# Performance work log

Measured on AMD Instinct MI355X. Metric: run time of the kernel, lower is better.

Reference implementation:

```python
import jax, jax.numpy as jnp
import numpy as np

I_P = 8  # input_patch == output_patch


def extract_patches(x, i_p=I_P):
    # x: (B, N, C, H, W) -> (r, N*i_p*i_p, B, C), matching nn.Unfold(i_p, 1, 0, i_p)
    # followed by rearrange '(b n) (c i) r -> r (n i) b c' with i = h*w row-major.
    B, N, C, H, W = x.shape
    s1, s2 = H // i_p, W // i_p
    p = x.reshape(B, N, C, s1, i_p, s2, i_p)
    p = jnp.transpose(p, (3, 5, 1, 4, 6, 0, 2))  # (s1, s2, N, ph, pw, B, C)
    return p.reshape(s1 * s2, N * i_p * i_p, B, C)


def setup_inputs() -> dict:
    key = jax.random.key(0)
    ks = jax.random.split(key, 8)
    B, N, C, H = 1, 5, 3, 256
    inputs = jax.random.normal(ks[0], (B, N, C, H, H), jnp.float32)
    outputs = jax.random.normal(ks[1], (B, N, C, H, H), jnp.float32)
    # q/k projections of nn.MultiheadAttention(3, 1); v_proj and out_proj are frozen identity.
    Wq = jax.random.normal(ks[2], (3, 3), jnp.float32) * 0.5
    Wk = jax.random.normal(ks[3], (3, 3), jnp.float32) * 0.5
    bq = jax.random.normal(ks[4], (3,), jnp.float32) * 0.05
    bk = jax.random.normal(ks[5], (3,), jnp.float32) * 0.05
    bv = jnp.zeros((3,), jnp.float32)  # in_proj_bias for v initialised to zero
    return {
        "inputs": inputs,
        "outputs": outputs,
        "Wq": Wq,
        "Wk": Wk,
        "bq": bq,
        "bk": bk,
        "bv": bv,
        "loss_diff": jnp.float32(0.5),
        "step": 10,
        "max_steps": 100,
    }


def reference(inputs, outputs, Wq, Wk, bq, bk, bv, loss_diff, step, max_steps):
    B, N, C, H, W = inputs.shape
    i_p = I_P
    s = H // i_p
    mid = N // 2

    # (r, L, 3) with L = N*i_p^2; batch dim B==1 squeezed.
    X = extract_patches(inputs)[:, :, 0, :]
    Y = extract_patches(outputs)[:, :, 0, :]

    # The per-frame attention calls concatenated over frames equal a single
    # self-attention with Q=K=V=in_patches_flat (softmax is row-wise in queries).
    q = (X @ Wq.T + bq) / jnp.sqrt(jnp.float32(3.0))  # head_dim = 3
    k = X @ Wk.T + bk
    v = X + bv  # v_proj is identity (frozen)
    scores = jnp.einsum("rld,rmd->rlm", q, k)          # (r, L, L)
    attn = jax.nn.softmax(scores, axis=-1)
    out = jnp.einsum("rlm,rmd->rld", attn, v)           # out_proj identity, bias 0

    r = out.shape[0]
    # '(n h w) bs d -> (bs n) d h w' with bs=1  ->  (r, N, 3, i_p, i_p)
    align = out.reshape(r, N, i_p, i_p, 3).transpose(0, 1, 4, 2, 3)
    nin = Y.reshape(r, N, i_p, i_p, 3).transpose(0, 1, 4, 2, 3)

    per_patch_mse = lambda a, b: jnp.mean((a - b) ** 2, axis=(1, 2, 3, 4))
    mid_loss = jnp.sum(per_patch_mse(jnp.broadcast_to(nin[:, mid:mid + 1], align.shape), align))
    all_loss = jnp.sum(per_patch_mse(nin, align))
    coeff = loss_diff * (1.0 - step / max_steps) ** 10

    rec = jnp.mean(align, axis=1)  # (r, 3, i_p, i_p)
    rec_image = rec.reshape(s, s, 3, i_p, i_p).transpose(2, 0, 3, 1, 4).reshape(1, 3, H, W)
    rec_loss = jnp.mean((outputs[:, mid] - rec_image) ** 2)

    loss = mid_loss + coeff * all_loss + rec_loss
    return loss, rec_image
```

## Files before the change

### kernel.cpp

```cpp
#include <hip/hip_runtime.h>

#define HW    256
#define PLANE (256*256)
#define L     320
#define MID   2
#define NF    5
#define KPW   80

__device__ __forceinline__ float hw_exp2(float x) {
#if __has_builtin(__builtin_amdgcn_exp2f)
    return __builtin_amdgcn_exp2f(x);
#else
    float r;
    asm("v_exp_f32 %0, %1" : "=v"(r) : "v"(x));
    return r;
#endif
}

__global__ __launch_bounds__(256, 4) void attn_patch_kernel(
    const float* __restrict__ in,
    const float* __restrict__ outp,
    const float* __restrict__ Wq,
    const float* __restrict__ Wk,
    const float* __restrict__ bq,
    const float* __restrict__ bk,
    const float* __restrict__ bv,
    const float* __restrict__ loss_diff,
    const int*   __restrict__ step,
    const int*   __restrict__ max_steps,
    float* __restrict__ d_out)
{
    __shared__ float4 ksh[L];
    __shared__ float4 vsh[L];
    __shared__ float4 red[3][NF][64];

    const int tid = threadIdx.x;
    const int w   = tid >> 6;
    const int l   = tid & 63;
    const int r   = blockIdx.x;
    const int s1  = r >> 5, s2 = r & 31;

    const float bv0 = bv[0], bv1 = bv[1], bv2 = bv[2];

    for (int t = tid; t < L; t += 256) {
        const int n = t >> 6, i = t & 63;
        const int pix = (s1 * 8 + (i >> 3)) * HW + s2 * 8 + (i & 7);
        const float x0 = in[(n * 3 + 0) * PLANE + pix];
        const float x1 = in[(n * 3 + 1) * PLANE + pix];
        const float x2 = in[(n * 3 + 2) * PLANE + pix];
        const float k0 = x0 * Wk[0] + x1 * Wk[1] + x2 * Wk[2] + bk[0];
        const float k1 = x0 * Wk[3] + x1 * Wk[4] + x2 * Wk[5] + bk[1];
        const float k2 = x0 * Wk[6] + x1 * Wk[7] + x2 * Wk[8] + bk[2];
        ksh[t] = make_float4(k0, k1, k2, 0.0f);
        vsh[t] = make_float4(x0 + bv0, x1 + bv1, x2 + bv2, 0.0f);
    }
    __syncthreads();

    const float QS = 0.57735026918962576f * 1.44269504088896340f;
    float q[NF][3];
#pragma unroll
    for (int n = 0; n < NF; ++n) {
        const float4 vv = vsh[n * 64 + l];
        const float x0 = vv.x - bv0, x1 = vv.y - bv1, x2 = vv.z - bv2;
        q[n][0] = (x0 * Wq[0] + x1 * Wq[1] + x2 * Wq[2] + bq[0]) * QS;
        q[n][1] = (x0 * Wq[3] + x1 * Wq[4] + x2 * Wq[5] + bq[1]) * QS;
        q[n][2] = (x0 * Wq[6] + x1 * Wq[7] + x2 * Wq[8] + bq[2]) * QS;
    }

    float den[NF] = {0, 0, 0, 0, 0};
    float acc[NF][3] = {};
    const int m0 = w * KPW;
#pragma unroll 4
    for (int mm = 0; mm < KPW; ++mm) {
        const int m = m0 + mm;
        const float4 kk = ksh[m];
        const float4 vv = vsh[m];
#pragma unroll
        for (int j = 0; j < NF; ++j) {
            const float s = q[j][0] * kk.x + q[j][1] * kk.y + q[j][2] * kk.z;
            const float p = hw_exp2(s);
            den[j]    += p;
            acc[j][0] += p * vv.x;
            acc[j][1] += p * vv.y;
            acc[j][2] += p * vv.z;
        }
    }

    if (w > 0) {
#pragma unroll
        for (int j = 0; j < NF; ++j)
            red[w - 1][j][l] = make_float4(acc[j][0], acc[j][1], acc[j][2], den[j]);
    }
    __syncthreads();
    if (w == 0) {
#pragma unroll
        for (int ww = 0; ww < 3; ++ww)
#pragma unroll
            for (int j = 0; j < NF; ++j) {
                const float4 p = red[ww][j][l];
                acc[j][0] += p.x; acc[j][1] += p.y; acc[j][2] += p.z; den[j] += p.w;
            }

        const int pix = (s1 * 8 + (l >> 3)) * HW + s2 * 8 + (l & 7);
        float o[NF][3];
#pragma unroll
        for (int j = 0; j < NF; ++j) {
            const float inv = 1.0f / den[j];
            o[j][0] = acc[j][0] * inv;
            o[j][1] = acc[j][1] * inv;
            o[j][2] = acc[j][2] * inv;
        }

        float y[NF][3];
#pragma unroll
        for (int j = 0; j < NF; ++j)
#pragma unroll
            for (int c = 0; c < 3; ++c)
                y[j][c] = outp[(j * 3 + c) * PLANE + pix];

        const float t  = 1.0f - (float)step[0] / (float)max_steps[0];
        const float t2 = t * t, t4 = t2 * t2, t8 = t4 * t4;
        const float coeff = loss_diff[0] * t8 * t2;

        float midp = 0.0f, allp = 0.0f;
#pragma unroll
        for (int j = 0; j < NF; ++j)
#pragma unroll
            for (int c = 0; c < 3; ++c) {
                const float d = y[MID][c] - o[j][c];
                const float e = y[j][c]   - o[j][c];
                midp += d * d;
                allp += e * e;
            }
        float tl = (midp + coeff * allp) * (1.0f / 960.0f);

#pragma unroll
        for (int c = 0; c < 3; ++c) {
            const float rec = 0.2f * (o[0][c] + o[1][c] + o[2][c] + o[3][c] + o[4][c]);
            d_out[1 + c * PLANE + pix] = rec;
            const float dr = y[MID][c] - rec;
            tl += dr * dr * (1.0f / 196608.0f);
        }

#pragma unroll
        for (int off = 32; off; off >>= 1) tl += __shfl_down(tl, off);
        if (l == 0) atomicAdd(d_out, tl);
    }
}

extern "C" void kernel_launch(void* const* d_in, const int* in_sizes, int n_in,
                              void* d_out, int out_size, void* d_ws, size_t ws_size,
                              hipStream_t stream) {
    const float* in        = (const float*)d_in[0];
    const float* outp      = (const float*)d_in[1];
    const float* Wq        = (const float*)d_in[2];
    const float* Wk        = (const float*)d_in[3];
    const float* bq        = (const float*)d_in[4];
    const float* bk        = (const float*)d_in[5];
    const float* bv        = (const float*)d_in[6];
    const float* loss_diff = (const float*)d_in[7];
    const int*   step      = (const int*)d_in[8];
    const int*   max_steps = (const int*)d_in[9];
    float* out = (float*)d_out;

    hipMemsetAsync(out, 0, sizeof(float), stream);

    attn_patch_kernel<<<1024, 256, 0, stream>>>(
        in, outp, Wq, Wk, bq, bk, bv, loss_diff, step, max_steps, out);
}
```

Baseline: 112.0 us.

## Pack key/value pairs into SoA shared layout and use packed float2 FMA

```diff
diff --git a/kernel.cpp b/kernel.cpp
--- a/kernel.cpp
+++ b/kernel.cpp
@@ -3,9 +3,12 @@
 #define HW    256
 #define PLANE (256*256)
 #define L     320
+#define NP    160
 #define MID   2
 #define NF    5
-#define KPW   80
+#define PPW   40
+
+typedef float v2f __attribute__((ext_vector_type(2)));
 
 __device__ __forceinline__ float hw_exp2(float x) {
 #if __has_builtin(__builtin_amdgcn_exp2f)
@@ -30,8 +33,9 @@
     const int*   __restrict__ max_steps,
     float* __restrict__ d_out)
 {
-    __shared__ float4 ksh[L];
-    __shared__ float4 vsh[L];
+    __shared__ float4 A[NP];
+    __shared__ float4 B[NP];
+    __shared__ float4 C[NP];
     __shared__ float4 red[3][NF][64];
 
     const int tid = threadIdx.x;
@@ -42,64 +46,97 @@
 
     const float bv0 = bv[0], bv1 = bv[1], bv2 = bv[2];
 
-    for (int t = tid; t < L; t += 256) {
-        const int n = t >> 6, i = t & 63;
-        const int pix = (s1 * 8 + (i >> 3)) * HW + s2 * 8 + (i & 7);
-        const float x0 = in[(n * 3 + 0) * PLANE + pix];
-        const float x1 = in[(n * 3 + 1) * PLANE + pix];
-        const float x2 = in[(n * 3 + 2) * PLANE + pix];
-        const float k0 = x0 * Wk[0] + x1 * Wk[1] + x2 * Wk[2] + bk[0];
-        const float k1 = x0 * Wk[3] + x1 * Wk[4] + x2 * Wk[5] + bk[1];
-        const float k2 = x0 * Wk[6] + x1 * Wk[7] + x2 * Wk[8] + bk[2];
-        ksh[t] = make_float4(k0, k1, k2, 0.0f);
-        vsh[t] = make_float4(x0 + bv0, x1 + bv1, x2 + bv2, 0.0f);
+    if (tid < NP) {
+        const int m0 = 2 * tid;
+        const int n  = m0 >> 6, i = m0 & 63;
+        const int ph = i >> 3, pw = i & 7;
+        const int pix = (s1 * 8 + ph) * HW + s2 * 8 + pw;
+        const float2 x0p = *(const float2*)&in[(n * 3 + 0) * PLANE + pix];
+        const float2 x1p = *(const float2*)&in[(n * 3 + 1) * PLANE + pix];
+        const float2 x2p = *(const float2*)&in[(n * 3 + 2) * PLANE + pix];
+        const float ka0 = x0p.x * Wk[0] + x1p.x * Wk[1] + x2p.x * Wk[2] + bk[0];
+        const float ka1 = x0p.x * Wk[3] + x1p.x * Wk[4] + x2p.x * Wk[5] + bk[1];
+        const float ka2 = x0p.x * Wk[6] + x1p.x * Wk[7] + x2p.x * Wk[8] + bk[2];
+        const float kb0 = x0p.y * Wk[0] + x1p.y * Wk[1] + x2p.y * Wk[2] + bk[0];
+        const float kb1 = x0p.y * Wk[3] + x1p.y * Wk[4] + x2p.y * Wk[5] + bk[1];
+        const float kb2 = x0p.y * Wk[6] + x1p.y * Wk[7] + x2p.y * Wk[8] + bk[2];
+        A[tid] = make_float4(ka0, kb0, ka1, kb1);
+        B[tid] = make_float4(ka2, kb2, x0p.x + bv0, x0p.y + bv0);
+        C[tid] = make_float4(x1p.x + bv1, x1p.y + bv1, x2p.x + bv2, x2p.y + bv2);
     }
     __syncthreads();
 
     const float QS = 0.57735026918962576f * 1.44269504088896340f;
-    float q[NF][3];
+    v2f qs[NF][3];
 #pragma unroll
     for (int n = 0; n < NF; ++n) {
-        const float4 vv = vsh[n * 64 + l];
-        const float x0 = vv.x - bv0, x1 = vv.y - bv1, x2 = vv.z - bv2;
-        q[n][0] = (x0 * Wq[0] + x1 * Wq[1] + x2 * Wq[2] + bq[0]) * QS;
-        q[n][1] = (x0 * Wq[3] + x1 * Wq[4] + x2 * Wq[5] + bq[1]) * QS;
-        q[n][2] = (x0 * Wq[6] + x1 * Wq[7] + x2 * Wq[8] + bq[2]) * QS;
-    }
-
-    float den[NF] = {0, 0, 0, 0, 0};
-    float acc[NF][3] = {};
-    const int m0 = w * KPW;
-#pragma unroll 4
-    for (int mm = 0; mm < KPW; ++mm) {
-        const int m = m0 + mm;
-        const float4 kk = ksh[m];
-        const float4 vv = vsh[m];
+        const int m  = n * 64 + l;
+        const int mm = m >> 1, h = m & 1;
+        const float4 b4 = B[mm];
+        const float4 c4 = C[mm];
+        const float x0 = (h ? b4.w : b4.z) - bv0;
+        const float x1 = (h ? c4.y : c4.x) - bv1;
+        const float x2 = (h ? c4.w : c4.z) - bv2;
+        const float q0 = (x0 * Wq[0] + x1 * Wq[1] + x2 * Wq[2] + bq[0]) * QS;
+        const float q1 = (x0 * Wq[3] + x1 * Wq[4] + x2 * Wq[5] + bq[1]) * QS;
+        const float q2 = (x0 * Wq[6] + x1 * Wq[7] + x2 * Wq[8] + bq[2]) * QS;
+        qs[n][0] = (v2f){q0, q0};
+        qs[n][1] = (v2f){q1, q1};
+        qs[n][2] = (v2f){q2, q2};
+    }
+
+    v2f den2[NF] = {};
+    v2f acc2[NF][3] = {};
+    const int p0 = w * PPW;
+#pragma unroll 2
+    for (int pp = 0; pp < PPW; ++pp) {
+        const float4 a4 = A[p0 + pp];
+        const float4 b4 = B[p0 + pp];
+        const float4 c4 = C[p0 + pp];
+        const v2f kx = (v2f){a4.x, a4.y};
+        const v2f ky = (v2f){a4.z, a4.w};
+        const v2f kz = (v2f){b4.x, b4.y};
+        const v2f vx = (v2f){b4.z, b4.w};
+        const v2f vy = (v2f){c4.x, c4.y};
+        const v2f vz = (v2f){c4.z, c4.w};
 #pragma unroll
         for (int j = 0; j < NF; ++j) {
-            const float s = q[j][0] * kk.x + q[j][1] * kk.y + q[j][2] * kk.z;
-            const float p = hw_exp2(s);
-            den[j]    += p;
-            acc[j][0] += p * vv.x;
-            acc[j][1] += p * vv.y;
-            acc[j][2] += p * vv.z;
+            v2f s = kx * qs[j][0];
+            s = __builtin_elementwise_fma(ky, qs[j][1], s);
+            s = __builtin_elementwise_fma(kz, qs[j][2], s);
+            v2f p;
+            p.x = hw_exp2(s.x);
+            p.y = hw_exp2(s.y);
+            den2[j] += p;
+            acc2[j][0] = __builtin_elementwise_fma(p, vx, acc2[j][0]);
+            acc2[j][1] = __builtin_elementwise_fma(p, vy, acc2[j][1]);
+            acc2[j][2] = __builtin_elementwise_fma(p, vz, acc2[j][2]);
         }
     }
 
     if (w > 0) {
 #pragma unroll
         for (int j = 0; j < NF; ++j)
-            red[w - 1][j][l] = make_float4(acc[j][0], acc[j][1], acc[j][2], den[j]);
+            red[w - 1][j][l] = make_float4(acc2[j][0].x + acc2[j][0].y,
+                                           acc2[j][1].x + acc2[j][1].y,
+                                           acc2[j][2].x + acc2[j][2].y,
+                                           den2[j].x + den2[j].y);
     }
     __syncthreads();
     if (w == 0) {
-#pragma unroll
-        for (int ww = 0; ww < 3; ++ww)
-#pragma unroll
-            for (int j = 0; j < NF; ++j) {
+        float den[NF], acc[NF][3];
+#pragma unroll
+        for (int j = 0; j < NF; ++j) {
+            den[j]    = den2[j].x + den2[j].y;
+            acc[j][0] = acc2[j][0].x + acc2[j][0].y;
+            acc[j][1] = acc2[j][1].x + acc2[j][1].y;
+            acc[j][2] = acc2[j][2].x + acc2[j][2].y;
+#pragma unroll
+            for (int ww = 0; ww < 3; ++ww) {
                 const float4 p = red[ww][j][l];
                 acc[j][0] += p.x; acc[j][1] += p.y; acc[j][2] += p.z; den[j] += p.w;
             }
+        }
 
         const int pix = (s1 * 8 + (l >> 3)) * HW + s2 * 8 + (l & 7);
         float o[NF][3];
```

Measured after the change: 104.3 us. -6.9%, faster.
